# Performance work log

Measured on AMD Instinct MI355X. Metric: run time of the kernel, lower is better.

The kernel has to match this reference:

```python
import jax, jax.numpy as jnp
import numpy as np

N = 100000   # total nodes across the ragged graph batch
E = 800000   # edges
B = 4096     # graphs
V = 103      # element vocab (embedding rows)
D_IN = 200   # embedding dim
H = 256      # hidden dim


def setup_inputs() -> dict:
    key = jax.random.key(0)
    ks = jax.random.split(key, 20)
    s = 0.05
    return {
        "weight": jax.random.normal(ks[0], (V, D_IN), jnp.float32),
        "sto_x": jax.random.randint(ks[1], (N,), 0, V),
        "sto_edge_index": jax.random.randint(ks[2], (2, E), 0, N),
        "sto_weight": jax.random.uniform(ks[3], (N,), jnp.float32),
        "sto_batch": jnp.sort(jax.random.randint(ks[4], (N,), 0, B)),
        "gW0": jax.random.normal(ks[5], (D_IN, H), jnp.float32) * s,
        "gb0": jnp.zeros((H,), jnp.float32),
        "gW1": jax.random.normal(ks[6], (H, H), jnp.float32) * s,
        "gb1": jnp.zeros((H,), jnp.float32),
        "gW2": jax.random.normal(ks[7], (H, H), jnp.float32) * s,
        "gb2": jnp.zeros((H,), jnp.float32),
        "lstm_Wih": jax.random.normal(ks[8], (4 * H, 2 * H), jnp.float32) * s,
        "lstm_Whh": jax.random.normal(ks[9], (4 * H, H), jnp.float32) * s,
        "lstm_bih": jnp.zeros((4 * H,), jnp.float32),
        "lstm_bhh": jnp.zeros((4 * H,), jnp.float32),
        "mlin_W": jax.random.normal(ks[10], (H, 2 * H), jnp.float32) * s,
        "mlin_b": jnp.zeros((H,), jnp.float32),
        "p0W": jax.random.normal(ks[11], (128, H), jnp.float32) * s,
        "p0b": jnp.zeros((128,), jnp.float32),
        "p1W": jax.random.normal(ks[12], (128, 128), jnp.float32) * s,
        "p1b": jnp.zeros((128,), jnp.float32),
        "p2W": jax.random.normal(ks[13], (1, 128), jnp.float32) * s,
        "p2b": jnp.zeros((1,), jnp.float32),
    }


def reference(weight, sto_x, sto_edge_index, sto_weight, sto_batch,
              gW0, gb0, gW1, gb1, gW2, gb2,
              lstm_Wih, lstm_Whh, lstm_bih, lstm_bhh,
              mlin_W, mlin_b, p0W, p0b, p1W, p1b, p2W, p2b):
    # embedding gather (sto_x - 1, with -1 wrapping to the last row as in torch)
    x = weight[sto_x - 1]

    # --- GCN (3 layers, symmetric norm with self-loops, ReLU between layers) ---
    loop = jnp.arange(N)
    src = jnp.concatenate([sto_edge_index[0], loop])
    dst = jnp.concatenate([sto_edge_index[1], loop])
    deg = jax.ops.segment_sum(jnp.ones_like(dst, jnp.float32), dst, N)
    dinv = jax.lax.rsqrt(jnp.maximum(deg, 1.0))
    norm = (dinv[src] * dinv[dst])[:, None]

    def conv(h_in, W, b):
        hw = h_in @ W                                   # [N, H]
        return jax.ops.segment_sum(hw[src] * norm, dst, N) + b

    x = jax.nn.relu(conv(x, gW0, gb0))
    x = jax.nn.relu(conv(x, gW1, gb1))
    x = conv(x, gW2, gb2)

    # --- stoichiometric weighting + graph-wise scatter sum ---
    wx = x * sto_weight[:, None]                        # [N, H]
    sto = jax.ops.segment_sum(wx, sto_batch, B)         # [B, H]

    # --- Set2Set pooling (2 processing steps, 1-layer LSTM) ---
    h = jnp.zeros((B, H), wx.dtype)
    c = jnp.zeros((B, H), wx.dtype)
    q_star = jnp.zeros((B, 2 * H), wx.dtype)
    for _ in range(2):
        gates = q_star @ lstm_Wih.T + lstm_bih + h @ lstm_Whh.T + lstm_bhh
        i, f, g, o = jnp.split(gates, 4, axis=-1)
        c = jax.nn.sigmoid(f) * c + jax.nn.sigmoid(i) * jnp.tanh(g)
        h = jax.nn.sigmoid(o) * jnp.tanh(c)
        e = jnp.sum(wx * h[sto_batch], axis=-1)         # [N]
        emax = jax.ops.segment_max(e, sto_batch, B)
        a = jnp.exp(e - emax[sto_batch])
        a = a / (jax.ops.segment_sum(a, sto_batch, B)[sto_batch] + 1e-16)
        r = jax.ops.segment_sum(wx * a[:, None], sto_batch, B)
        q_star = jnp.concatenate([h, r], axis=-1)

    mean = q_star @ mlin_W.T + mlin_b + sto
    mean = mean / jnp.maximum(jnp.linalg.norm(mean, axis=1, keepdims=True), 1e-12)

    # --- predictor MLP (LeakyReLU slope 0.01) ---
    y = jax.nn.leaky_relu(mean @ p0W.T + p0b)
    y = jax.nn.leaky_relu(y @ p1W.T + p1b)
    return y @ p2W.T + p2b                              # [B, 1]
```

## Files before the change

kernel.cpp:

```cpp
#include <hip/hip_runtime.h>
#include <math.h>

constexpr int Nn  = 100000;
constexpr int Ee  = 800000;
constexpr int Bb  = 4096;
constexpr int Vv  = 103;
constexpr int DIN = 200;
constexpr int Hh  = 256;
constexpr int KV  = 128;

constexpr int SCHUNK = 1024;
constexpr int NSCAN  = (Nn + SCHUNK - 1)/SCHUNK;

using short8 = __attribute__((ext_vector_type(8))) short;
using f32x4  = __attribute__((ext_vector_type(4))) float;

__device__ __forceinline__ float sigf(float x){ return 1.f/(1.f+expf(-x)); }

__device__ __forceinline__ unsigned short f2bf(float f){
  unsigned int u = __float_as_uint(f);
  u += 0x7FFFu + ((u >> 16) & 1u);
  return (unsigned short)(u >> 16);
}
__device__ __forceinline__ float bf2f(unsigned int u){
  return __uint_as_float((u & 0xFFFFu) << 16);
}

__global__ void k_transpose(const float* __restrict__ in, float* __restrict__ out, int R, int C){
  int idx = blockIdx.x*256 + threadIdx.x;
  if (idx >= R*C) return;
  int r = idx / C, c = idx % C;
  out[(size_t)c*R + r] = in[(size_t)r*C + c];
}

__global__ void k_transpose_b(const float* __restrict__ in, unsigned short* __restrict__ out, int R, int C){
  int idx = blockIdx.x*256 + threadIdx.x;
  if (idx >= R*C) return;
  int r = idx / C, c = idx % C;
  out[(size_t)c*R + r] = f2bf(in[(size_t)r*C + c]);
}

__global__ void k_castb(const float* __restrict__ in, unsigned short* __restrict__ out, int n){
  int i = blockIdx.x*256 + threadIdx.x;
  if (i < n) out[i] = f2bf(in[i]);
}

__global__ void k_wg0t(const float* __restrict__ WG0, unsigned short* __restrict__ WG0tb){
  int i = blockIdx.x*256 + threadIdx.x;
  if (i >= Hh*KV) return;
  int n = i >> 7, k = i & (KV-1);
  float v = (k < Vv) ? WG0[(size_t)k*Hh + n] : 0.f;
  WG0tb[i] = f2bf(v);
}

__global__ void k_packW(const float* __restrict__ Wih, const float* __restrict__ Whh,
                        unsigned short* __restrict__ Wp){
  int i = blockIdx.x*256 + threadIdx.x;
  if (i >= 4*Hh*3*Hh) return;
  int g = i / (3*Hh), j = i % (3*Hh);
  float v = (j < 2*Hh) ? Wih[(size_t)g*2*Hh + j] : Whh[(size_t)g*Hh + (j - 2*Hh)];
  Wp[i] = f2bf(v);
}

__global__ void k_count(const int* __restrict__ dst, int* __restrict__ counts){
  int e = blockIdx.x*256 + threadIdx.x;
  if (e < Ee) atomicAdd(&counts[dst[e]], 1);
}

__global__ void k_dinv(const int* __restrict__ counts, float* __restrict__ dinv){
  int n = blockIdx.x*256 + threadIdx.x;
  if (n < Nn) dinv[n] = rsqrtf((float)(counts[n] + 1));
}

__global__ void k_scan1(const int* __restrict__ counts, int* __restrict__ partial){
  __shared__ int red[256];
  int t = threadIdx.x;
  int base = blockIdx.x*SCHUNK + t*4;
  int s = 0;
  if (base + 3 < Nn){ int4 v = *reinterpret_cast<const int4*>(counts + base); s = v.x+v.y+v.z+v.w; }
  else { for (int i=0;i<4;++i) if (base+i<Nn) s += counts[base+i]; }
  red[t] = s; __syncthreads();
  for (int st=128; st>0; st>>=1){ if (t<st) red[t]+=red[t+st]; __syncthreads(); }
  if (t==0) partial[blockIdx.x] = red[0];
}

__global__ void k_scan2(int* __restrict__ partial, int n){
  __shared__ int buf[128];
  int t = threadIdx.x;
  int v = (t < n) ? partial[t] : 0;
  buf[t] = v; __syncthreads();
  for (int off=1; off<128; off<<=1){
    int tv = (t>=off) ? buf[t-off] : 0;
    __syncthreads();
    buf[t] += tv;
    __syncthreads();
  }
  if (t < n) partial[t] = buf[t] - v;
}

__global__ void k_scan3(const int* __restrict__ counts, const int* __restrict__ partial,
                        int* __restrict__ offs){
  __shared__ int red[256];
  int t = threadIdx.x;
  int base = blockIdx.x*SCHUNK + t*4;
  int c0=0,c1=0,c2=0,c3=0;
  if (base + 3 < Nn){ int4 v = *reinterpret_cast<const int4*>(counts + base); c0=v.x;c1=v.y;c2=v.z;c3=v.w; }
  else { if (base<Nn) c0=counts[base]; if (base+1<Nn) c1=counts[base+1];
         if (base+2<Nn) c2=counts[base+2]; if (base+3<Nn) c3=counts[base+3]; }
  int s = c0+c1+c2+c3;
  red[t] = s; __syncthreads();
  for (int off=1; off<256; off<<=1){
    int tv = (t>=off) ? red[t-off] : 0;
    __syncthreads();
    red[t] += tv;
    __syncthreads();
  }
  int run = partial[blockIdx.x] + red[t] - s;
  if (base   < Nn) offs[base]   = run; run += c0;
  if (base+1 < Nn) offs[base+1] = run; run += c1;
  if (base+2 < Nn) offs[base+2] = run; run += c2;
  if (base+3 < Nn) offs[base+3] = run; run += c3;
  if (blockIdx.x == gridDim.x-1 && t == 255) offs[Nn] = partial[blockIdx.x] + red[255];
}

__global__ void k_copyi(const int* __restrict__ a, int* __restrict__ b, int n){
  int i = blockIdx.x*256 + threadIdx.x;
  if (i < n) b[i] = a[i];
}

__global__ void k_fill(const int* __restrict__ ei, const float* __restrict__ dinv,
                       int* __restrict__ fptr, int* __restrict__ srcs, float* __restrict__ norms){
  int e = blockIdx.x*256 + threadIdx.x;
  if (e >= Ee) return;
  int s = ei[e], d = ei[Ee + e];
  int pos = atomicAdd(&fptr[d], 1);
  srcs[pos]  = s;
  norms[pos] = dinv[s]*dinv[d];
}

__global__ void k_boffs(const int* __restrict__ batch, int* __restrict__ boffs){
  int b = blockIdx.x*256 + threadIdx.x;
  if (b > Bb) return;
  int lo = 0, hi = Nn;
  while (lo < hi){ int mid = (lo+hi)>>1; if (batch[mid] < b) lo = mid+1; else hi = mid; }
  boffs[b] = lo;
}

__global__ void k_hist(const int* __restrict__ sto_x, const int* __restrict__ offs,
                       const int* __restrict__ srcs, const float* __restrict__ norms,
                       const float* __restrict__ dinv, unsigned short* __restrict__ Vb){
  __shared__ float hist[4][KV];
  int wid = threadIdx.x >> 6, lane = threadIdx.x & 63;
  int n = blockIdx.x*4 + wid;
  hist[wid][lane] = 0.f; hist[wid][lane+64] = 0.f;
  __syncthreads();
  int s = offs[n], e = offs[n+1];
  for (int k = s + lane; k < e; k += 64){
    int r2 = sto_x[srcs[k]]; r2 = (r2 == 0) ? (Vv-1) : r2-1;
    atomicAdd(&hist[wid][r2], norms[k]);
  }
  if (lane == 0){
    int r0 = sto_x[n]; r0 = (r0 == 0) ? (Vv-1) : r0-1;
    float dn = dinv[n];
    atomicAdd(&hist[wid][r0], dn*dn);
  }
  __syncthreads();
  unsigned int p = ((unsigned int)f2bf(hist[wid][2*lane+1]) << 16) | f2bf(hist[wid][2*lane]);
  ((unsigned int*)Vb)[(size_t)n*(KV/2) + lane] = p;
}

__global__ void k_agg(const unsigned short* __restrict__ Xb, const int* __restrict__ offs,
                      const int* __restrict__ srcs, const float* __restrict__ norms,
                      const float* __restrict__ dinv, unsigned short* __restrict__ T){
  int wid = threadIdx.x >> 6, lane = threadIdx.x & 63;
  int n = blockIdx.x*4 + wid;
  const uint2* Xv = (const uint2*)Xb;
  uint2 v = Xv[(size_t)n*64 + lane];
  float dn = dinv[n]; float s2 = dn*dn;
  float a0 = bf2f(v.x)*s2, a1 = bf2f(v.x>>16)*s2;
  float a2 = bf2f(v.y)*s2, a3 = bf2f(v.y>>16)*s2;
  int s = offs[n], e = offs[n+1];
  int k = s;
  for (; k + 3 < e; k += 4){
    int s0 = srcs[k], s1 = srcs[k+1], s2i = srcs[k+2], s3 = srcs[k+3];
    float n0 = norms[k], n1 = norms[k+1], n2 = norms[k+2], n3 = norms[k+3];
    uint2 g0 = Xv[(size_t)s0*64 + lane];
    uint2 g1 = Xv[(size_t)s1*64 + lane];
    uint2 g2 = Xv[(size_t)s2i*64 + lane];
    uint2 g3 = Xv[(size_t)s3*64 + lane];
    a0 += bf2f(g0.x)*n0; a1 += bf2f(g0.x>>16)*n0; a2 += bf2f(g0.y)*n0; a3 += bf2f(g0.y>>16)*n0;
    a0 += bf2f(g1.x)*n1; a1 += bf2f(g1.x>>16)*n1; a2 += bf2f(g1.y)*n1; a3 += bf2f(g1.y>>16)*n1;
    a0 += bf2f(g2.x)*n2; a1 += bf2f(g2.x>>16)*n2; a2 += bf2f(g2.y)*n2; a3 += bf2f(g2.y>>16)*n2;
    a0 += bf2f(g3.x)*n3; a1 += bf2f(g3.x>>16)*n3; a2 += bf2f(g3.y)*n3; a3 += bf2f(g3.y>>16)*n3;
  }
  for (; k < e; ++k){
    uint2 g0 = Xv[(size_t)srcs[k]*64 + lane];
    float n0 = norms[k];
    a0 += bf2f(g0.x)*n0; a1 += bf2f(g0.x>>16)*n0;
    a2 += bf2f(g0.y)*n0; a3 += bf2f(g0.y>>16)*n0;
  }
  uint2 o;
  o.x = (unsigned int)f2bf(a0) | ((unsigned int)f2bf(a1) << 16);
  o.y = (unsigned int)f2bf(a2) | ((unsigned int)f2bf(a3) << 16);
  ((uint2*)T)[(size_t)n*64 + lane] = o;
}

__global__ __launch_bounds__(512) void k_gemm8(
    const unsigned short* __restrict__ A, int lda,
    const unsigned short* __restrict__ Bt,
    const float* __restrict__ bias, const float* __restrict__ rowscale,
    const float* __restrict__ addf,
    float* __restrict__ Cf, unsigned short* __restrict__ Cb,
    int M, int K, int Nc, int relu)
{
  __shared__ unsigned short lds[18432];
  unsigned short (*Al)[40] = (unsigned short(*)[40])lds;
  unsigned short (*Bl)[40] = (unsigned short(*)[40])(lds + 128*40);

  int tid = threadIdx.x;
  int w = tid >> 6, lane = tid & 63;
  int wr = (w >> 1)*32, wc = (w & 1)*64;
  int l16 = lane & 15, kh = lane >> 4;
  int rbase = blockIdx.y*128, cbase = blockIdx.x*128;
  int sr = tid >> 2, sb = tid & 3;

  f32x4 acc[2][4] = {};

  for (int k0 = 0; k0 < K; k0 += 32){
    int kk = k0 + sb*8;
    uint4 a0 = make_uint4(0,0,0,0);
    int ar0 = rbase + sr;
    if (ar0 < M) a0 = *reinterpret_cast<const uint4*>(A + (size_t)ar0*lda + kk);
    uint4 b0 = *reinterpret_cast<const uint4*>(Bt + (size_t)(cbase + sr)*K + kk);
    __syncthreads();
    *reinterpret_cast<uint4*>(&Al[sr][sb*8]) = a0;
    *reinterpret_cast<uint4*>(&Bl[sr][sb*8]) = b0;
    __syncthreads();

    short8 af[2], bfv[4];
    #pragma unroll
    for (int m = 0; m < 2; ++m) af[m] = *reinterpret_cast<const short8*>(&Al[wr + m*16 + l16][kh*8]);
    #pragma unroll
    for (int n2 = 0; n2 < 4; ++n2) bfv[n2] = *reinterpret_cast<const short8*>(&Bl[wc + n2*16 + l16][kh*8]);
    #pragma unroll
    for (int m = 0; m < 2; ++m)
      #pragma unroll
      for (int n2 = 0; n2 < 4; ++n2)
        acc[m][n2] = __builtin_amdgcn_mfma_f32_16x16x32_bf16(af[m], bfv[n2], acc[m][n2], 0, 0, 0);
  }

  if (Cf){
    #pragma unroll
    for (int n2 = 0; n2 < 4; ++n2){
      int col = cbase + wc + n2*16 + l16;
      float bv = bias ? bias[col] : 0.f;
      #pragma unroll
      for (int m = 0; m < 2; ++m){
        #pragma unroll
        for (int i = 0; i < 4; ++i){
          int row = rbase + wr + m*16 + kh*4 + i;
          if (row >= M) continue;
          float v = acc[m][n2][i] + bv;
          if (addf) v += addf[(size_t)row*Nc + col];
          if (rowscale) v *= rowscale[row];
          if (relu) v = fmaxf(v, 0.f);
          Cf[(size_t)row*Nc + col] = v;
        }
      }
    }
  }
  if (Cb){
    __syncthreads();
    unsigned short* eps = lds + w*(32*72);
    #pragma unroll
    for (int n2 = 0; n2 < 4; ++n2){
      int colg = cbase + wc + n2*16 + l16;
      float bv = bias ? bias[colg] : 0.f;
      #pragma unroll
      for (int m = 0; m < 2; ++m){
        #pragma unroll
        for (int i = 0; i < 4; ++i){
          int lrow = m*16 + kh*4 + i;
          int rowg = rbase + wr + lrow;
          float v = acc[m][n2][i] + bv;
          float rs = (rowscale && rowg < M) ? rowscale[rowg] : 1.f;
          v *= rs;
          if (relu) v = fmaxf(v, 0.f);
          eps[lrow*72 + n2*16 + l16] = f2bf(v);
        }
      }
    }
    int c8 = lane & 7;
    #pragma unroll
    for (int rd = 0; rd < 4; ++rd){
      int lrow = rd*8 + (lane >> 3);
      int rowg = rbase + wr + lrow;
      short8 vv = *reinterpret_cast<const short8*>(&eps[lrow*72 + c8*8]);
      if (rowg < M)
        *reinterpret_cast<short8*>(Cb + (size_t)rowg*Nc + cbase + wc + c8*8) = vv;
    }
  }
}

__global__ __launch_bounds__(256) void k_gemm_nt(
    const float* __restrict__ A, const float* __restrict__ Bt,
    const float* __restrict__ bias, const float* __restrict__ Dadd,
    float* __restrict__ C, int M, int K, int Nc, int accum, int act)
{
  __shared__ float As[64][20];
  __shared__ float Bs[64][20];
  int tid = threadIdx.x;
  int rbase = blockIdx.y*64, cbase = blockIdx.x*64;
  int ty = tid>>4, tx = tid&15;
  int lr = tid>>2, lq = tid&3;
  float acc[4][4] = {};
  for (int k0 = 0; k0 < K; k0 += 16){
    float4 av = make_float4(0,0,0,0), bv = make_float4(0,0,0,0);
    int kk = k0 + lq*4;
    int ar = rbase + lr;
    if (ar < M && kk < K){
      if (kk + 3 < K) av = *reinterpret_cast<const float4*>(A + (size_t)ar*K + kk);
      else { float t0[4] = {0,0,0,0}; for (int i=0; i<4 && kk+i<K; ++i) t0[i] = A[(size_t)ar*K + kk + i];
             av = make_float4(t0[0],t0[1],t0[2],t0[3]); }
    }
    int br = cbase + lr;
    if (br < Nc && kk < K){
      if (kk + 3 < K) bv = *reinterpret_cast<const float4*>(Bt + (size_t)br*K + kk);
      else { float t0[4] = {0,0,0,0}; for (int i=0; i<4 && kk+i<K; ++i) t0[i] = Bt[(size_t)br*K + kk + i];
             bv = make_float4(t0[0],t0[1],t0[2],t0[3]); }
    }
    __syncthreads();
    *reinterpret_cast<float4*>(&As[lr][lq*4]) = av;
    *reinterpret_cast<float4*>(&Bs[lr][lq*4]) = bv;
    __syncthreads();
    #pragma unroll
    for (int kc = 0; kc < 16; kc += 4){
      float4 a4[4], b4[4];
      #pragma unroll
      for (int i=0;i<4;++i) a4[i] = *reinterpret_cast<float4*>(&As[ty*4+i][kc]);
      #pragma unroll
      for (int j=0;j<4;++j) b4[j] = *reinterpret_cast<float4*>(&Bs[tx*4+j][kc]);
      #pragma unroll
      for (int i=0;i<4;++i)
        #pragma unroll
        for (int j=0;j<4;++j)
          acc[i][j] += a4[i].x*b4[j].x + a4[i].y*b4[j].y + a4[i].z*b4[j].z + a4[i].w*b4[j].w;
    }
  }
  #pragma unroll
  for (int i=0;i<4;++i){
    int r = rbase + ty*4 + i;
    if (r >= M) continue;
    #pragma unroll
    for (int j=0;j<4;++j){
      int cc = cbase + tx*4 + j;
      if (cc >= Nc) continue;
      float v = acc[i][j];
      if (accum) v += C[(size_t)r*Nc + cc];
      if (bias)  v += bias[cc];
      if (Dadd)  v += Dadd[(size_t)r*Nc + cc];
      if (act == 1) v = (v > 0.f) ? v : 0.01f*v;
      C[(size_t)r*Nc + cc] = v;
    }
  }
}

__global__ void k_bsum(const float* __restrict__ bih, const float* __restrict__ bhh,
                       float* __restrict__ bsum){
  int g = blockIdx.x*256 + threadIdx.x;
  if (g < 4*Hh) bsum[g] = bih[g] + bhh[g];
}

__global__ void k_lstm(const float* __restrict__ gates, float* __restrict__ cbuf,
                       float* __restrict__ hbuf, unsigned short* __restrict__ qh){
  int idx = blockIdx.x*256 + threadIdx.x;
  if (idx >= Bb*Hh) return;
  int b = idx >> 8, ch = idx & 255;
  const float* g = gates + (size_t)b*4*Hh;
  float ig = sigf(g[ch]);
  float fg = sigf(g[Hh + ch]);
  float gg = tanhf(g[2*Hh + ch]);
  float og = sigf(g[3*Hh + ch]);
  float cn = fg*cbuf[idx] + ig*gg;
  float hn = og*tanhf(cn);
  cbuf[idx] = cn; hbuf[idx] = hn;
  unsigned short hb = f2bf(hn);
  qh[(size_t)b*3*Hh + ch] = hb;
  qh[(size_t)b*3*Hh + 2*Hh + ch] = hb;
}

__global__ void k_pool(const unsigned short* __restrict__ wxb,
                       const float* __restrict__ hbuf,
                       const int* __restrict__ boffs,
                       unsigned short* __restrict__ qh,
                       float* __restrict__ sto, int do_sto){
  int wid = threadIdx.x >> 6, lane = threadIdx.x & 63;
  int g = blockIdx.x*4 + wid;
  if (g >= Bb) return;
  const uint2* Xv = (const uint2*)wxb;
  float4 hv = ((const float4*)hbuf)[(size_t)g*64 + lane];
  int s = boffs[g], e = boffs[g+1];
  float m = -INFINITY, ssum = 0.f;
  float a0=0.f,a1=0.f,a2=0.f,a3=0.f;
  float t0=0.f,t1=0.f,t2=0.f,t3=0.f;
  for (int n = s; n < e; ++n){
    uint2 v = Xv[(size_t)n*64 + lane];
    float x0=bf2f(v.x), x1=bf2f(v.x>>16), x2=bf2f(v.y), x3=bf2f(v.y>>16);
    if (do_sto){ t0+=x0; t1+=x1; t2+=x2; t3+=x3; }
    float d = x0*hv.x + x1*hv.y + x2*hv.z + x3*hv.w;
    #pragma unroll
    for (int mask=32; mask; mask>>=1) d += __shfl_xor(d, mask, 64);
    if (d > m){
      float sc = expf(m - d);
      ssum = ssum*sc + 1.f;
      a0 = a0*sc + x0; a1 = a1*sc + x1; a2 = a2*sc + x2; a3 = a3*sc + x3;
      m = d;
    } else {
      float p = expf(d - m);
      ssum += p;
      a0 += p*x0; a1 += p*x1; a2 += p*x2; a3 += p*x3;
    }
  }
  float inv = 1.f/(ssum + 1e-16f);
  uint2 o;
  o.x = (unsigned int)f2bf(a0*inv) | ((unsigned int)f2bf(a1*inv) << 16);
  o.y = (unsigned int)f2bf(a2*inv) | ((unsigned int)f2bf(a3*inv) << 16);
  ((uint2*)(qh + (size_t)g*3*Hh + Hh))[lane] = o;
  if (do_sto) ((float4*)sto)[(size_t)g*64 + lane] = make_float4(t0,t1,t2,t3);
}

__global__ void k_norm(float* __restrict__ mean){
  __shared__ float red[256];
  int b = blockIdx.x, tid = threadIdx.x;
  float v = mean[(size_t)b*Hh + tid];
  red[tid] = v*v; __syncthreads();
  for (int st=128; st>0; st>>=1){ if (tid<st) red[tid] += red[tid+st]; __syncthreads(); }
  float nrm = fmaxf(sqrtf(red[0]), 1e-12f);
  mean[(size_t)b*Hh + tid] = v/nrm;
}

__global__ void k_out(const float* __restrict__ y1, const float* __restrict__ p2W,
                      const float* __restrict__ p2b, float* __restrict__ out){
  __shared__ float red[128];
  int b = blockIdx.x, tid = threadIdx.x;
  float v = y1[(size_t)b*128 + tid]*p2W[tid];
  red[tid] = v; __syncthreads();
  for (int st=64; st>0; st>>=1){ if (tid<st) red[tid] += red[tid+st]; __syncthreads(); }
  if (tid == 0) out[b] = red[0] + p2b[0];
}

extern "C" void kernel_launch(void* const* d_in, const int* in_sizes, int n_in,
                              void* d_out, int out_size, void* d_ws, size_t ws_size,
                              hipStream_t stream) {
  const float* weight   = (const float*)d_in[0];
  const int*   sto_x    = (const int*)  d_in[1];
  const int*   ei       = (const int*)  d_in[2];
  const float* sto_w    = (const float*)d_in[3];
  const int*   batch    = (const int*)  d_in[4];
  const float* gW0 = (const float*)d_in[5];   const float* gb0 = (const float*)d_in[6];
  const float* gW1 = (const float*)d_in[7];   const float* gb1 = (const float*)d_in[8];
  const float* gW2 = (const float*)d_in[9];   const float* gb2 = (const float*)d_in[10];
  const float* Wih = (const float*)d_in[11];  const float* Whh = (const float*)d_in[12];
  const float* bih = (const float*)d_in[13];  const float* bhh = (const float*)d_in[14];
  const float* mW  = (const float*)d_in[15];  const float* mb  = (const float*)d_in[16];
  const float* p0W = (const float*)d_in[17];  const float* p0b = (const float*)d_in[18];
  const float* p1W = (const float*)d_in[19];  const float* p1b = (const float*)d_in[20];
  const float* p2W = (const float*)d_in[21];  const float* p2b = (const float*)d_in[22];
  float* out = (float*)d_out;

  char* w = (char*)d_ws;
  auto alloc = [&](size_t bytes)->char*{ char* p = w; w += (bytes + 255) & ~size_t(255); return p; };
  unsigned short* Xb = (unsigned short*)alloc((size_t)Nn*Hh*2);
  unsigned short* Tb = (unsigned short*)alloc((size_t)Nn*Hh*2);
  unsigned short* Vb = (unsigned short*)alloc((size_t)Nn*KV*2);
  float* WG0   = (float*)alloc((size_t)Vv*Hh*4);
  unsigned short* WG0tb = (unsigned short*)alloc((size_t)Hh*KV*2);
  float* gW0t  = (float*)alloc((size_t)Hh*DIN*4);
  unsigned short* gW1tb = (unsigned short*)alloc((size_t)Hh*Hh*2);
  unsigned short* gW2tb = (unsigned short*)alloc((size_t)Hh*Hh*2);
  unsigned short* Wpb   = (unsigned short*)alloc((size_t)4*Hh*3*Hh*2);
  unsigned short* mWb   = (unsigned short*)alloc((size_t)Hh*2*Hh*2);
  int*   counts= (int*)  alloc((size_t)Nn*4);
  int*   offs  = (int*)  alloc((size_t)(Nn+1)*4);
  int*   fptr  = (int*)  alloc((size_t)Nn*4);
  int*   spart = (int*)  alloc((size_t)NSCAN*4);
  float* dinv  = (float*)alloc((size_t)Nn*4);
  int*   srcs  = (int*)  alloc((size_t)Ee*4);
  float* norms = (float*)alloc((size_t)Ee*4);
  int*   boffs = (int*)  alloc((size_t)(Bb+1)*4);
  float* sto   = (float*)alloc((size_t)Bb*Hh*4);
  float* hbuf  = (float*)alloc((size_t)Bb*Hh*4);
  float* cbuf  = (float*)alloc((size_t)Bb*Hh*4);
  unsigned short* qh = (unsigned short*)alloc((size_t)Bb*3*Hh*2);
  float* gates = (float*)alloc((size_t)Bb*4*Hh*4);
  float* bsum  = (float*)alloc((size_t)4*Hh*4);
  float* meanb = (float*)alloc((size_t)Bb*Hh*4);
  float* y0    = (float*)alloc((size_t)Bb*128*4);
  float* y1    = (float*)alloc((size_t)Bb*128*4);

  auto gemm = [&](const float* A, const float* Bt, const float* bias, const float* Dadd,
                  float* C, int M, int K, int Nc, int accum, int act){
    dim3 g((Nc+63)/64, (M+63)/64);
    k_gemm_nt<<<g, 256, 0, stream>>>(A, Bt, bias, Dadd, C, M, K, Nc, accum, act);
  };
  auto gemm8 = [&](const unsigned short* A, int lda, const unsigned short* Bt,
                   const float* bias, const float* rowscale, const float* addf,
                   float* Cf, unsigned short* Cb, int M, int K, int Nc, int relu){
    dim3 g(Nc/128, (M+127)/128);
    k_gemm8<<<g, 512, 0, stream>>>(A, lda, Bt, bias, rowscale, addf, Cf, Cb, M, K, Nc, relu);
  };

  hipMemsetAsync(counts, 0, (size_t)Nn*4, stream);
  hipMemsetAsync(cbuf,  0, (size_t)Bb*Hh*4, stream);
  hipMemsetAsync(qh,    0, (size_t)Bb*3*Hh*2, stream);

  k_transpose<<<(DIN*Hh+255)/256, 256, 0, stream>>>(gW0, gW0t, DIN, Hh);
  k_transpose_b<<<(Hh*Hh+255)/256, 256, 0, stream>>>(gW1, gW1tb, Hh, Hh);
  k_transpose_b<<<(Hh*Hh+255)/256, 256, 0, stream>>>(gW2, gW2tb, Hh, Hh);
  k_packW<<<(4*Hh*3*Hh+255)/256, 256, 0, stream>>>(Wih, Whh, Wpb);
  k_castb<<<(Hh*2*Hh+255)/256, 256, 0, stream>>>(mW, mWb, Hh*2*Hh);

  k_count<<<(Ee+255)/256, 256, 0, stream>>>(ei + Ee, counts);
  k_dinv<<<(Nn+255)/256, 256, 0, stream>>>(counts, dinv);
  k_scan1<<<NSCAN, 256, 0, stream>>>(counts, spart);
  k_scan2<<<1, 128, 0, stream>>>(spart, NSCAN);
  k_scan3<<<NSCAN, 256, 0, stream>>>(counts, spart, offs);
  k_copyi<<<(Nn+255)/256, 256, 0, stream>>>(offs, fptr, Nn);
  k_fill<<<(Ee+255)/256, 256, 0, stream>>>(ei, dinv, fptr, srcs, norms);
  k_boffs<<<(Bb+256)/256, 256, 0, stream>>>(batch, boffs);

  gemm(weight, gW0t, nullptr, nullptr, WG0, Vv, DIN, Hh, 0, 0);
  k_wg0t<<<(Hh*KV+255)/256, 256, 0, stream>>>(WG0, WG0tb);
  k_hist<<<Nn/4, 256, 0, stream>>>(sto_x, offs, srcs, norms, dinv, Vb);
  gemm8(Vb, KV, WG0tb, gb0, nullptr, nullptr, nullptr, Xb, Nn, KV, Hh, 1);

  k_agg<<<Nn/4, 256, 0, stream>>>(Xb, offs, srcs, norms, dinv, Tb);
  gemm8(Tb, Hh, gW1tb, gb1, nullptr, nullptr, nullptr, Xb, Nn, Hh, Hh, 1);
  k_agg<<<Nn/4, 256, 0, stream>>>(Xb, offs, srcs, norms, dinv, Tb);
  gemm8(Tb, Hh, gW2tb, gb2, sto_w, nullptr, nullptr, Xb, Nn, Hh, Hh, 0);

  k_bsum<<<(4*Hh+255)/256, 256, 0, stream>>>(bih, bhh, bsum);

  for (int t = 0; t < 2; ++t){
    gemm8(qh, 3*Hh, Wpb, bsum, nullptr, nullptr, gates, nullptr, Bb, 3*Hh, 4*Hh, 0);
    k_lstm<<<(Bb*Hh+255)/256, 256, 0, stream>>>(gates, cbuf, hbuf, qh);
    k_pool<<<Bb/4, 256, 0, stream>>>(Xb, hbuf, boffs, qh, sto, t == 0);
  }

  gemm8(qh, 3*Hh, mWb, mb, nullptr, sto, meanb, nullptr, Bb, 2*Hh, Hh, 0);
  k_norm<<<Bb, Hh, 0, stream>>>(meanb);
  gemm(meanb, p0W, p0b, nullptr, y0, Bb, Hh, 128, 0, 1);
  gemm(y0, p1W, p1b, nullptr, y1, Bb, 128, 128, 0, 1);
  k_out<<<Bb, 128, 0, stream>>>(y1, p2W, p2b, out);
}
```

Measured before the change: 593.0 us.

## Fuse GCN aggregation with layer GEMM, pack edge records, move MLP to bf16 MFMA

Merges the neighbor aggregation and the following dense 256x256 GEMM into one kernel for GCN layers 2 and 3. Each block aggregates 64 rows into LDS and multiplies them with MFMA, so the bf16 intermediate T no longer makes a round trip through global memory. Edge source index and norm are packed into one uint2 so each edge needs a single load. The predictor MLP now runs through the bf16 MFMA GEMM with a LeakyReLU mode instead of fp32 GEMMs, which costs some precision in that head. The fused kernel reads its B operand straight from global memory (L2) rather than staging it in LDS.

```diff
diff --git a/kernel.cpp b/kernel.cpp
--- a/kernel.cpp
+++ b/kernel.cpp
@@ -129,13 +129,12 @@
 }
 
 __global__ void k_fill(const int* __restrict__ ei, const float* __restrict__ dinv,
-                       int* __restrict__ fptr, int* __restrict__ srcs, float* __restrict__ norms){
+                       int* __restrict__ fptr, uint2* __restrict__ epack){
   int e = blockIdx.x*256 + threadIdx.x;
   if (e >= Ee) return;
   int s = ei[e], d = ei[Ee + e];
   int pos = atomicAdd(&fptr[d], 1);
-  srcs[pos]  = s;
-  norms[pos] = dinv[s]*dinv[d];
+  epack[pos] = make_uint2((unsigned int)s, __float_as_uint(dinv[s]*dinv[d]));
 }
 
 __global__ void k_boffs(const int* __restrict__ batch, int* __restrict__ boffs){
@@ -147,8 +146,8 @@
 }
 
 __global__ void k_hist(const int* __restrict__ sto_x, const int* __restrict__ offs,
-                       const int* __restrict__ srcs, const float* __restrict__ norms,
-                       const float* __restrict__ dinv, unsigned short* __restrict__ Vb){
+                       const uint2* __restrict__ epack, const float* __restrict__ dinv,
+                       unsigned short* __restrict__ Vb){
   __shared__ float hist[4][KV];
   int wid = threadIdx.x >> 6, lane = threadIdx.x & 63;
   int n = blockIdx.x*4 + wid;
@@ -156,8 +155,9 @@
   __syncthreads();
   int s = offs[n], e = offs[n+1];
   for (int k = s + lane; k < e; k += 64){
-    int r2 = sto_x[srcs[k]]; r2 = (r2 == 0) ? (Vv-1) : r2-1;
-    atomicAdd(&hist[wid][r2], norms[k]);
+    uint2 ev = epack[k];
+    int r2 = sto_x[ev.x]; r2 = (r2 == 0) ? (Vv-1) : r2-1;
+    atomicAdd(&hist[wid][r2], __uint_as_float(ev.y));
   }
   if (lane == 0){
     int r0 = sto_x[n]; r0 = (r0 == 0) ? (Vv-1) : r0-1;
@@ -169,40 +169,111 @@
   ((unsigned int*)Vb)[(size_t)n*(KV/2) + lane] = p;
 }
 
-__global__ void k_agg(const unsigned short* __restrict__ Xb, const int* __restrict__ offs,
-                      const int* __restrict__ srcs, const float* __restrict__ norms,
-                      const float* __restrict__ dinv, unsigned short* __restrict__ T){
-  int wid = threadIdx.x >> 6, lane = threadIdx.x & 63;
-  int n = blockIdx.x*4 + wid;
+__global__ __launch_bounds__(512, 4) void k_conv_fused(
+    const unsigned short* __restrict__ Xb,
+    const uint2* __restrict__ epack,
+    const int* __restrict__ offs,
+    const float* __restrict__ dinv,
+    const unsigned short* __restrict__ Bt,
+    const float* __restrict__ bias,
+    const float* __restrict__ sw,
+    unsigned short* __restrict__ Cb,
+    int M, int relu)
+{
+  __shared__ unsigned short lds[18432];
+  unsigned short (*Tl)[264] = (unsigned short(*)[264])lds;
+
+  int tid = threadIdx.x;
+  int w = tid >> 6, lane = tid & 63;
+  int rbase = blockIdx.x * 64;
   const uint2* Xv = (const uint2*)Xb;
-  uint2 v = Xv[(size_t)n*64 + lane];
-  float dn = dinv[n]; float s2 = dn*dn;
-  float a0 = bf2f(v.x)*s2, a1 = bf2f(v.x>>16)*s2;
-  float a2 = bf2f(v.y)*s2, a3 = bf2f(v.y>>16)*s2;
-  int s = offs[n], e = offs[n+1];
-  int k = s;
-  for (; k + 3 < e; k += 4){
-    int s0 = srcs[k], s1 = srcs[k+1], s2i = srcs[k+2], s3 = srcs[k+3];
-    float n0 = norms[k], n1 = norms[k+1], n2 = norms[k+2], n3 = norms[k+3];
-    uint2 g0 = Xv[(size_t)s0*64 + lane];
-    uint2 g1 = Xv[(size_t)s1*64 + lane];
-    uint2 g2 = Xv[(size_t)s2i*64 + lane];
-    uint2 g3 = Xv[(size_t)s3*64 + lane];
-    a0 += bf2f(g0.x)*n0; a1 += bf2f(g0.x>>16)*n0; a2 += bf2f(g0.y)*n0; a3 += bf2f(g0.y>>16)*n0;
-    a0 += bf2f(g1.x)*n1; a1 += bf2f(g1.x>>16)*n1; a2 += bf2f(g1.y)*n1; a3 += bf2f(g1.y>>16)*n1;
-    a0 += bf2f(g2.x)*n2; a1 += bf2f(g2.x>>16)*n2; a2 += bf2f(g2.y)*n2; a3 += bf2f(g2.y>>16)*n2;
-    a0 += bf2f(g3.x)*n3; a1 += bf2f(g3.x>>16)*n3; a2 += bf2f(g3.y)*n3; a3 += bf2f(g3.y>>16)*n3;
-  }
-  for (; k < e; ++k){
-    uint2 g0 = Xv[(size_t)srcs[k]*64 + lane];
-    float n0 = norms[k];
-    a0 += bf2f(g0.x)*n0; a1 += bf2f(g0.x>>16)*n0;
-    a2 += bf2f(g0.y)*n0; a3 += bf2f(g0.y>>16)*n0;
-  }
-  uint2 o;
-  o.x = (unsigned int)f2bf(a0) | ((unsigned int)f2bf(a1) << 16);
-  o.y = (unsigned int)f2bf(a2) | ((unsigned int)f2bf(a3) << 16);
-  ((uint2*)T)[(size_t)n*64 + lane] = o;
+
+  for (int i = 0; i < 8; ++i){
+    int lr = w*8 + i;
+    int n = rbase + lr;
+    if (n >= M) break;
+    float dn = dinv[n]; float s2 = dn*dn;
+    uint2 v = Xv[(size_t)n*64 + lane];
+    float a0 = bf2f(v.x)*s2, a1 = bf2f(v.x>>16)*s2;
+    float a2 = bf2f(v.y)*s2, a3 = bf2f(v.y>>16)*s2;
+    int s = offs[n], e = offs[n+1];
+    int k = s;
+    for (; k + 3 < e; k += 4){
+      uint2 e0 = epack[k], e1 = epack[k+1], e2 = epack[k+2], e3 = epack[k+3];
+      uint2 g0 = Xv[(size_t)e0.x*64 + lane];
+      uint2 g1 = Xv[(size_t)e1.x*64 + lane];
+      uint2 g2 = Xv[(size_t)e2.x*64 + lane];
+      uint2 g3 = Xv[(size_t)e3.x*64 + lane];
+      float n0 = __uint_as_float(e0.y), n1 = __uint_as_float(e1.y);
+      float n2 = __uint_as_float(e2.y), n3 = __uint_as_float(e3.y);
+      a0 += bf2f(g0.x)*n0; a1 += bf2f(g0.x>>16)*n0; a2 += bf2f(g0.y)*n0; a3 += bf2f(g0.y>>16)*n0;
+      a0 += bf2f(g1.x)*n1; a1 += bf2f(g1.x>>16)*n1; a2 += bf2f(g1.y)*n1; a3 += bf2f(g1.y>>16)*n1;
+      a0 += bf2f(g2.x)*n2; a1 += bf2f(g2.x>>16)*n2; a2 += bf2f(g2.y)*n2; a3 += bf2f(g2.y>>16)*n2;
+      a0 += bf2f(g3.x)*n3; a1 += bf2f(g3.x>>16)*n3; a2 += bf2f(g3.y)*n3; a3 += bf2f(g3.y>>16)*n3;
+    }
+    for (; k < e; ++k){
+      uint2 e0 = epack[k];
+      uint2 g0 = Xv[(size_t)e0.x*64 + lane];
+      float n0 = __uint_as_float(e0.y);
+      a0 += bf2f(g0.x)*n0; a1 += bf2f(g0.x>>16)*n0;
+      a2 += bf2f(g0.y)*n0; a3 += bf2f(g0.y>>16)*n0;
+    }
+    uint2 o;
+    o.x = (unsigned int)f2bf(a0) | ((unsigned int)f2bf(a1) << 16);
+    o.y = (unsigned int)f2bf(a2) | ((unsigned int)f2bf(a3) << 16);
+    *reinterpret_cast<uint2*>(&Tl[lr][lane*4]) = o;
+  }
+  __syncthreads();
+
+  int l16 = lane & 15, kh = lane >> 4;
+  int wr = (w >> 2)*32, wc = (w & 3)*64;
+  f32x4 acc[2][4] = {};
+  const unsigned short* bp0 = Bt + (size_t)(wc + l16)*256 + kh*8;
+
+  #pragma unroll
+  for (int kk = 0; kk < 8; ++kk){
+    short8 af0 = *reinterpret_cast<const short8*>(&Tl[wr + l16][kk*32 + kh*8]);
+    short8 af1 = *reinterpret_cast<const short8*>(&Tl[wr + 16 + l16][kk*32 + kh*8]);
+    short8 bs[4];
+    #pragma unroll
+    for (int f = 0; f < 4; ++f)
+      bs[f] = *reinterpret_cast<const short8*>(bp0 + (size_t)f*16*256 + kk*32);
+    #pragma unroll
+    for (int f = 0; f < 4; ++f){
+      acc[0][f] = __builtin_amdgcn_mfma_f32_16x16x32_bf16(af0, bs[f], acc[0][f], 0, 0, 0);
+      acc[1][f] = __builtin_amdgcn_mfma_f32_16x16x32_bf16(af1, bs[f], acc[1][f], 0, 0, 0);
+    }
+  }
+  __syncthreads();
+
+  unsigned short* eps = lds + w*(32*72);
+  #pragma unroll
+  for (int n2 = 0; n2 < 4; ++n2){
+    int col = wc + n2*16 + l16;
+    float bv = bias[col];
+    #pragma unroll
+    for (int m = 0; m < 2; ++m){
+      #pragma unroll
+      for (int i = 0; i < 4; ++i){
+        int lrow = m*16 + kh*4 + i;
+        int rowg = rbase + wr + lrow;
+        float v = acc[m][n2][i] + bv;
+        float rs = (sw && rowg < M) ? sw[rowg] : 1.f;
+        v *= rs;
+        if (relu) v = fmaxf(v, 0.f);
+        eps[lrow*72 + n2*16 + l16] = f2bf(v);
+      }
+    }
+  }
+  int c8 = lane & 7;
+  #pragma unroll
+  for (int rd = 0; rd < 4; ++rd){
+    int lrow = rd*8 + (lane >> 3);
+    int rowg = rbase + wr + lrow;
+    short8 vv = *reinterpret_cast<const short8*>(&eps[lrow*72 + c8*8]);
+    if (rowg < M)
+      *reinterpret_cast<short8*>(Cb + (size_t)rowg*256 + wc + c8*8) = vv;
+  }
 }
 
 __global__ __launch_bounds__(512) void k_gemm8(
@@ -263,7 +334,8 @@
           float v = acc[m][n2][i] + bv;
           if (addf) v += addf[(size_t)row*Nc + col];
           if (rowscale) v *= rowscale[row];
-          if (relu) v = fmaxf(v, 0.f);
+          if (relu == 1) v = fmaxf(v, 0.f);
+          else if (relu == 2) v = (v > 0.f) ? v : 0.01f*v;
           Cf[(size_t)row*Nc + col] = v;
         }
       }
@@ -285,7 +357,8 @@
           float v = acc[m][n2][i] + bv;
           float rs = (rowscale && rowg < M) ? rowscale[rowg] : 1.f;
           v *= rs;
-          if (relu) v = fmaxf(v, 0.f);
+          if (relu == 1) v = fmaxf(v, 0.f);
+          else if (relu == 2) v = (v > 0.f) ? v : 0.01f*v;
           eps[lrow*72 + n2*16 + l16] = f2bf(v);
         }
       }
@@ -429,14 +502,15 @@
   if (do_sto) ((float4*)sto)[(size_t)g*64 + lane] = make_float4(t0,t1,t2,t3);
 }
 
-__global__ void k_norm(float* __restrict__ mean){
+__global__ void k_norm(float* __restrict__ mean, unsigned short* __restrict__ outb){
   __shared__ float red[256];
   int b = blockIdx.x, tid = threadIdx.x;
   float v = mean[(size_t)b*Hh + tid];
   red[tid] = v*v; __syncthreads();
   for (int st=128; st>0; st>>=1){ if (tid<st) red[tid] += red[tid+st]; __syncthreads(); }
   float nrm = fmaxf(sqrtf(red[0]), 1e-12f);
-  mean[(size_t)b*Hh + tid] = v/nrm;
+  float o = v/nrm;
+  outb[(size_t)b*Hh + tid] = f2bf(o);
 }
 
 __global__ void k_out(const float* __restrict__ y1, const float* __restrict__ p2W,
@@ -470,8 +544,8 @@
 
   char* w = (char*)d_ws;
   auto alloc = [&](size_t bytes)->char*{ char* p = w; w += (bytes + 255) & ~size_t(255); return p; };
-  unsigned short* Xb = (unsigned short*)alloc((size_t)Nn*Hh*2);
-  unsigned short* Tb = (unsigned short*)alloc((size_t)Nn*Hh*2);
+  unsigned short* X1 = (unsigned short*)alloc((size_t)Nn*Hh*2);
+  unsigned short* X2 = (unsigned short*)alloc((size_t)Nn*Hh*2);
   unsigned short* Vb = (unsigned short*)alloc((size_t)Nn*KV*2);
   float* WG0   = (float*)alloc((size_t)Vv*Hh*4);
   unsigned short* WG0tb = (unsigned short*)alloc((size_t)Hh*KV*2);
@@ -480,13 +554,14 @@
   unsigned short* gW2tb = (unsigned short*)alloc((size_t)Hh*Hh*2);
   unsigned short* Wpb   = (unsigned short*)alloc((size_t)4*Hh*3*Hh*2);
   unsigned short* mWb   = (unsigned short*)alloc((size_t)Hh*2*Hh*2);
+  unsigned short* p0Wb  = (unsigned short*)alloc((size_t)128*Hh*2);
+  unsigned short* p1Wb  = (unsigned short*)alloc((size_t)128*128*2);
   int*   counts= (int*)  alloc((size_t)Nn*4);
   int*   offs  = (int*)  alloc((size_t)(Nn+1)*4);
   int*   fptr  = (int*)  alloc((size_t)Nn*4);
   int*   spart = (int*)  alloc((size_t)NSCAN*4);
   float* dinv  = (float*)alloc((size_t)Nn*4);
-  int*   srcs  = (int*)  alloc((size_t)Ee*4);
-  float* norms = (float*)alloc((size_t)Ee*4);
+  uint2* epack = (uint2*)alloc((size_t)Ee*8);
   int*   boffs = (int*)  alloc((size_t)(Bb+1)*4);
   float* sto   = (float*)alloc((size_t)Bb*Hh*4);
   float* hbuf  = (float*)alloc((size_t)Bb*Hh*4);
@@ -495,7 +570,8 @@
   float* gates = (float*)alloc((size_t)Bb*4*Hh*4);
   float* bsum  = (float*)alloc((size_t)4*Hh*4);
   float* meanb = (float*)alloc((size_t)Bb*Hh*4);
-  float* y0    = (float*)alloc((size_t)Bb*128*4);
+  unsigned short* meanbb = (unsigned short*)alloc((size_t)Bb*Hh*2);
+  unsigned short* y0b = (unsigned short*)alloc((size_t)Bb*128*2);
   float* y1    = (float*)alloc((size_t)Bb*128*4);
 
   auto gemm = [&](const float* A, const float* Bt, const float* bias, const float* Dadd,
@@ -519,6 +595,8 @@
   k_transpose_b<<<(Hh*Hh+255)/256, 256, 0, stream>>>(gW2, gW2tb, Hh, Hh);
   k_packW<<<(4*Hh*3*Hh+255)/256, 256, 0, stream>>>(Wih, Whh, Wpb);
   k_castb<<<(Hh*2*Hh+255)/256, 256, 0, stream>>>(mW, mWb, Hh*2*Hh);
+  k_castb<<<(128*Hh+255)/256, 256, 0, stream>>>(p0W, p0Wb, 128*Hh);
+  k_castb<<<(128*128+255)/256, 256, 0, stream>>>(p1W, p1Wb, 128*128);
 
   k_count<<<(Ee+255)/256, 256, 0, stream>>>(ei + Ee, counts);
   k_dinv<<<(Nn+255)/256, 256, 0, stream>>>(counts, dinv);
@@ -526,30 +604,28 @@
   k_scan2<<<1, 128, 0, stream>>>(spart, NSCAN);
   k_scan3<<<NSCAN, 256, 0, stream>>>(counts, spart, offs);
   k_copyi<<<(Nn+255)/256, 256, 0, stream>>>(offs, fptr, Nn);
-  k_fill<<<(Ee+255)/256, 256, 0, stream>>>(ei, dinv, fptr, srcs, norms);
+  k_fill<<<(Ee+255)/256, 256, 0, stream>>>(ei, dinv, fptr, epack);
   k_boffs<<<(Bb+256)/256, 256, 0, stream>>>(batch, boffs);
 
   gemm(weight, gW0t, nullptr, nullptr, WG0, Vv, DIN, Hh, 0, 0);
   k_wg0t<<<(Hh*KV+255)/256, 256, 0, stream>>>(WG0, WG0tb);
-  k_hist<<<Nn/4, 256, 0, stream>>>(sto_x, offs, srcs, norms, dinv, Vb);
-  gemm8(Vb, KV, WG0tb, gb0, nullptr, nullptr, nullptr, Xb, Nn, KV, Hh, 1);
-
-  k_agg<<<Nn/4, 256, 0, stream>>>(Xb, offs, srcs, norms, dinv, Tb);
-  gemm8(Tb, Hh, gW1tb, gb1, nullptr, nullptr, nullptr, Xb, Nn, Hh, Hh, 1);
-  k_agg<<<Nn/4, 256, 0, stream>>>(Xb, offs, srcs, norms, dinv, Tb);
-  gemm8(Tb, Hh, gW2tb, gb2, sto_w, nullptr, nullptr, Xb, Nn, Hh, Hh, 0);
+  k_hist<<<Nn/4, 256, 0, stream>>>(sto_x, offs, epack, dinv, Vb);
+  gemm8(Vb, KV, WG0tb, gb0, nullptr, nullptr, nullptr, X1, Nn, KV, Hh, 1);
+
+  k_conv_fused<<<(Nn+63)/64, 512, 0, stream>>>(X1, epack, offs, dinv, gW1tb, gb1, nullptr, X2, Nn, 1);
+  k_conv_fused<<<(Nn+63)/64, 512, 0, stream>>>(X2, epack, offs, dinv, gW2tb, gb2, sto_w, X1, Nn, 0);
 
   k_bsum<<<(4*Hh+255)/256, 256, 0, stream>>>(bih, bhh, bsum);
 
   for (int t = 0; t < 2; ++t){
     gemm8(qh, 3*Hh, Wpb, bsum, nullptr, nullptr, gates, nullptr, Bb, 3*Hh, 4*Hh, 0);
     k_lstm<<<(Bb*Hh+255)/256, 256, 0, stream>>>(gates, cbuf, hbuf, qh);
-    k_pool<<<Bb/4, 256, 0, stream>>>(Xb, hbuf, boffs, qh, sto, t == 0);
+    k_pool<<<Bb/4, 256, 0, stream>>>(X1, hbuf, boffs, qh, sto, t == 0);
   }
 
   gemm8(qh, 3*Hh, mWb, mb, nullptr, sto, meanb, nullptr, Bb, 2*Hh, Hh, 0);
-  k_norm<<<Bb, Hh, 0, stream>>>(meanb);
-  gemm(meanb, p0W, p0b, nullptr, y0, Bb, Hh, 128, 0, 1);
-  gemm(y0, p1W, p1b, nullptr, y1, Bb, 128, 128, 0, 1);
+  k_norm<<<Bb, Hh, 0, stream>>>(meanb, meanbb);
+  gemm8(meanbb, Hh, p0Wb, p0b, nullptr, nullptr, nullptr, y0b, Bb, Hh, 128, 2);
+  gemm8(y0b, 128, p1Wb, p1b, nullptr, nullptr, y1, nullptr, Bb, 128, 128, 2);
   k_out<<<Bb, 128, 0, stream>>>(y1, p2W, p2b, out);
 }
```

After: 688.4 us. 16.1% more time.

## Pack edge src/norm into uint2, unroll aggregation by 8, bf16 MFMA predictor MLP

Applied to the files above, without the earlier changes.

Source index and normalization weight are interleaved into one 8-byte record, so the aggregation and histogram kernels issue one load per edge instead of two. The aggregation loop now prefetches 8 edges and their feature gathers per iteration to raise memory-level parallelism. The two predictor MLP layers move from the fp32 GEMM to the bf16 MFMA GEMM, which gains a LeakyReLU mode; the normalized mean is written as bf16 and two extra weight casts are added. This lowers precision in the head and adds register pressure in the aggregation kernel.

```diff
diff --git a/kernel.cpp b/kernel.cpp
--- a/kernel.cpp
+++ b/kernel.cpp
@@ -129,13 +129,12 @@
 }
 
 __global__ void k_fill(const int* __restrict__ ei, const float* __restrict__ dinv,
-                       int* __restrict__ fptr, int* __restrict__ srcs, float* __restrict__ norms){
+                       int* __restrict__ fptr, uint2* __restrict__ epack){
   int e = blockIdx.x*256 + threadIdx.x;
   if (e >= Ee) return;
   int s = ei[e], d = ei[Ee + e];
   int pos = atomicAdd(&fptr[d], 1);
-  srcs[pos]  = s;
-  norms[pos] = dinv[s]*dinv[d];
+  epack[pos] = make_uint2((unsigned int)s, __float_as_uint(dinv[s]*dinv[d]));
 }
 
 __global__ void k_boffs(const int* __restrict__ batch, int* __restrict__ boffs){
@@ -147,8 +146,8 @@
 }
 
 __global__ void k_hist(const int* __restrict__ sto_x, const int* __restrict__ offs,
-                       const int* __restrict__ srcs, const float* __restrict__ norms,
-                       const float* __restrict__ dinv, unsigned short* __restrict__ Vb){
+                       const uint2* __restrict__ epack, const float* __restrict__ dinv,
+                       unsigned short* __restrict__ Vb){
   __shared__ float hist[4][KV];
   int wid = threadIdx.x >> 6, lane = threadIdx.x & 63;
   int n = blockIdx.x*4 + wid;
@@ -156,8 +155,9 @@
   __syncthreads();
   int s = offs[n], e = offs[n+1];
   for (int k = s + lane; k < e; k += 64){
-    int r2 = sto_x[srcs[k]]; r2 = (r2 == 0) ? (Vv-1) : r2-1;
-    atomicAdd(&hist[wid][r2], norms[k]);
+    uint2 ev = epack[k];
+    int r2 = sto_x[ev.x]; r2 = (r2 == 0) ? (Vv-1) : r2-1;
+    atomicAdd(&hist[wid][r2], __uint_as_float(ev.y));
   }
   if (lane == 0){
     int r0 = sto_x[n]; r0 = (r0 == 0) ? (Vv-1) : r0-1;
@@ -170,8 +170,8 @@
 }
 
 __global__ void k_agg(const unsigned short* __restrict__ Xb, const int* __restrict__ offs,
-                      const int* __restrict__ srcs, const float* __restrict__ norms,
-                      const float* __restrict__ dinv, unsigned short* __restrict__ T){
+                      const uint2* __restrict__ epack, const float* __restrict__ dinv,
+                      unsigned short* __restrict__ T){
   int wid = threadIdx.x >> 6, lane = threadIdx.x & 63;
   int n = blockIdx.x*4 + wid;
   const uint2* Xv = (const uint2*)Xb;
@@ -181,21 +181,31 @@
   float a2 = bf2f(v.y)*s2, a3 = bf2f(v.y>>16)*s2;
   int s = offs[n], e = offs[n+1];
   int k = s;
-  for (; k + 3 < e; k += 4){
-    int s0 = srcs[k], s1 = srcs[k+1], s2i = srcs[k+2], s3 = srcs[k+3];
-    float n0 = norms[k], n1 = norms[k+1], n2 = norms[k+2], n3 = norms[k+3];
-    uint2 g0 = Xv[(size_t)s0*64 + lane];
-    uint2 g1 = Xv[(size_t)s1*64 + lane];
-    uint2 g2 = Xv[(size_t)s2i*64 + lane];
-    uint2 g3 = Xv[(size_t)s3*64 + lane];
+  for (; k + 7 < e; k += 8){
+    uint2 ev[8], g[8];
+    #pragma unroll
+    for (int j = 0; j < 8; ++j) ev[j] = epack[k+j];
+    #pragma unroll
+    for (int j = 0; j < 8; ++j) g[j] = Xv[(size_t)ev[j].x*64 + lane];
+    #pragma unroll
+    for (int j = 0; j < 8; ++j){
+      float nn = __uint_as_float(ev[j].y);
+      a0 += bf2f(g[j].x)*nn; a1 += bf2f(g[j].x>>16)*nn;
+      a2 += bf2f(g[j].y)*nn; a3 += bf2f(g[j].y>>16)*nn;
+    }
+  }
+  for (; k + 1 < e; k += 2){
+    uint2 e0 = epack[k], e1 = epack[k+1];
+    uint2 g0 = Xv[(size_t)e0.x*64 + lane];
+    uint2 g1 = Xv[(size_t)e1.x*64 + lane];
+    float n0 = __uint_as_float(e0.y), n1 = __uint_as_float(e1.y);
     a0 += bf2f(g0.x)*n0; a1 += bf2f(g0.x>>16)*n0; a2 += bf2f(g0.y)*n0; a3 += bf2f(g0.y>>16)*n0;
     a0 += bf2f(g1.x)*n1; a1 += bf2f(g1.x>>16)*n1; a2 += bf2f(g1.y)*n1; a3 += bf2f(g1.y>>16)*n1;
-    a0 += bf2f(g2.x)*n2; a1 += bf2f(g2.x>>16)*n2; a2 += bf2f(g2.y)*n2; a3 += bf2f(g2.y>>16)*n2;
-    a0 += bf2f(g3.x)*n3; a1 += bf2f(g3.x>>16)*n3; a2 += bf2f(g3.y)*n3; a3 += bf2f(g3.y>>16)*n3;
-  }
-  for (; k < e; ++k){
-    uint2 g0 = Xv[(size_t)srcs[k]*64 + lane];
-    float n0 = norms[k];
+  }
+  if (k < e){
+    uint2 e0 = epack[k];
+    uint2 g0 = Xv[(size_t)e0.x*64 + lane];
+    float n0 = __uint_as_float(e0.y);
     a0 += bf2f(g0.x)*n0; a1 += bf2f(g0.x>>16)*n0;
     a2 += bf2f(g0.y)*n0; a3 += bf2f(g0.y>>16)*n0;
   }
@@ -263,7 +273,8 @@
           float v = acc[m][n2][i] + bv;
           if (addf) v += addf[(size_t)row*Nc + col];
           if (rowscale) v *= rowscale[row];
-          if (relu) v = fmaxf(v, 0.f);
+          if (relu == 1) v = fmaxf(v, 0.f);
+          else if (relu == 2) v = (v > 0.f) ? v : 0.01f*v;
           Cf[(size_t)row*Nc + col] = v;
         }
       }
@@ -285,7 +296,8 @@
           float v = acc[m][n2][i] + bv;
           float rs = (rowscale && rowg < M) ? rowscale[rowg] : 1.f;
           v *= rs;
-          if (relu) v = fmaxf(v, 0.f);
+          if (relu == 1) v = fmaxf(v, 0.f);
+          else if (relu == 2) v = (v > 0.f) ? v : 0.01f*v;
           eps[lrow*72 + n2*16 + l16] = f2bf(v);
         }
       }
@@ -429,14 +441,15 @@
   if (do_sto) ((float4*)sto)[(size_t)g*64 + lane] = make_float4(t0,t1,t2,t3);
 }
 
-__global__ void k_norm(float* __restrict__ mean){
+__global__ void k_norm(float* __restrict__ mean, unsigned short* __restrict__ outb){
   __shared__ float red[256];
   int b = blockIdx.x, tid = threadIdx.x;
   float v = mean[(size_t)b*Hh + tid];
   red[tid] = v*v; __syncthreads();
   for (int st=128; st>0; st>>=1){ if (tid<st) red[tid] += red[tid+st]; __syncthreads(); }
   float nrm = fmaxf(sqrtf(red[0]), 1e-12f);
-  mean[(size_t)b*Hh + tid] = v/nrm;
+  float o = v/nrm;
+  outb[(size_t)b*Hh + tid] = f2bf(o);
 }
 
 __global__ void k_out(const float* __restrict__ y1, const float* __restrict__ p2W,
@@ -480,13 +493,14 @@
   unsigned short* gW2tb = (unsigned short*)alloc((size_t)Hh*Hh*2);
   unsigned short* Wpb   = (unsigned short*)alloc((size_t)4*Hh*3*Hh*2);
   unsigned short* mWb   = (unsigned short*)alloc((size_t)Hh*2*Hh*2);
+  unsigned short* p0Wb  = (unsigned short*)alloc((size_t)128*Hh*2);
+  unsigned short* p1Wb  = (unsigned short*)alloc((size_t)128*128*2);
   int*   counts= (int*)  alloc((size_t)Nn*4);
   int*   offs  = (int*)  alloc((size_t)(Nn+1)*4);
   int*   fptr  = (int*)  alloc((size_t)Nn*4);
   int*   spart = (int*)  alloc((size_t)NSCAN*4);
   float* dinv  = (float*)alloc((size_t)Nn*4);
-  int*   srcs  = (int*)  alloc((size_t)Ee*4);
-  float* norms = (float*)alloc((size_t)Ee*4);
+  uint2* epack = (uint2*)alloc((size_t)Ee*8);
   int*   boffs = (int*)  alloc((size_t)(Bb+1)*4);
   float* sto   = (float*)alloc((size_t)Bb*Hh*4);
   float* hbuf  = (float*)alloc((size_t)Bb*Hh*4);
@@ -495,7 +509,8 @@
   float* gates = (float*)alloc((size_t)Bb*4*Hh*4);
   float* bsum  = (float*)alloc((size_t)4*Hh*4);
   float* meanb = (float*)alloc((size_t)Bb*Hh*4);
-  float* y0    = (float*)alloc((size_t)Bb*128*4);
+  unsigned short* meanbb = (unsigned short*)alloc((size_t)Bb*Hh*2);
+  unsigned short* y0b = (unsigned short*)alloc((size_t)Bb*128*2);
   float* y1    = (float*)alloc((size_t)Bb*128*4);
 
   auto gemm = [&](const float* A, const float* Bt, const float* bias, const float* Dadd,
@@ -519,6 +534,8 @@
   k_transpose_b<<<(Hh*Hh+255)/256, 256, 0, stream>>>(gW2, gW2tb, Hh, Hh);
   k_packW<<<(4*Hh*3*Hh+255)/256, 256, 0, stream>>>(Wih, Whh, Wpb);
   k_castb<<<(Hh*2*Hh+255)/256, 256, 0, stream>>>(mW, mWb, Hh*2*Hh);
+  k_castb<<<(128*Hh+255)/256, 256, 0, stream>>>(p0W, p0Wb, 128*Hh);
+  k_castb<<<(128*128+255)/256, 256, 0, stream>>>(p1W, p1Wb, 128*128);
 
   k_count<<<(Ee+255)/256, 256, 0, stream>>>(ei + Ee, counts);
   k_dinv<<<(Nn+255)/256, 256, 0, stream>>>(counts, dinv);
@@ -526,17 +543,17 @@
   k_scan2<<<1, 128, 0, stream>>>(spart, NSCAN);
   k_scan3<<<NSCAN, 256, 0, stream>>>(counts, spart, offs);
   k_copyi<<<(Nn+255)/256, 256, 0, stream>>>(offs, fptr, Nn);
-  k_fill<<<(Ee+255)/256, 256, 0, stream>>>(ei, dinv, fptr, srcs, norms);
+  k_fill<<<(Ee+255)/256, 256, 0, stream>>>(ei, dinv, fptr, epack);
   k_boffs<<<(Bb+256)/256, 256, 0, stream>>>(batch, boffs);
 
   gemm(weight, gW0t, nullptr, nullptr, WG0, Vv, DIN, Hh, 0, 0);
   k_wg0t<<<(Hh*KV+255)/256, 256, 0, stream>>>(WG0, WG0tb);
-  k_hist<<<Nn/4, 256, 0, stream>>>(sto_x, offs, srcs, norms, dinv, Vb);
+  k_hist<<<Nn/4, 256, 0, stream>>>(sto_x, offs, epack, dinv, Vb);
   gemm8(Vb, KV, WG0tb, gb0, nullptr, nullptr, nullptr, Xb, Nn, KV, Hh, 1);
 
-  k_agg<<<Nn/4, 256, 0, stream>>>(Xb, offs, srcs, norms, dinv, Tb);
+  k_agg<<<Nn/4, 256, 0, stream>>>(Xb, offs, epack, dinv, Tb);
   gemm8(Tb, Hh, gW1tb, gb1, nullptr, nullptr, nullptr, Xb, Nn, Hh, Hh, 1);
-  k_agg<<<Nn/4, 256, 0, stream>>>(Xb, offs, srcs, norms, dinv, Tb);
+  k_agg<<<Nn/4, 256, 0, stream>>>(Xb, offs, epack, dinv, Tb);
   gemm8(Tb, Hh, gW2tb, gb2, sto_w, nullptr, nullptr, Xb, Nn, Hh, Hh, 0);
 
   k_bsum<<<(4*Hh+255)/256, 256, 0, stream>>>(bih, bhh, bsum);
@@ -548,8 +565,8 @@
   }
 
   gemm8(qh, 3*Hh, mWb, mb, nullptr, sto, meanb, nullptr, Bb, 2*Hh, Hh, 0);
-  k_norm<<<Bb, Hh, 0, stream>>>(meanb);
-  gemm(meanb, p0W, p0b, nullptr, y0, Bb, Hh, 128, 0, 1);
-  gemm(y0, p1W, p1b, nullptr, y1, Bb, 128, 128, 0, 1);
+  k_norm<<<Bb, Hh, 0, stream>>>(meanb, meanbb);
+  gemm8(meanbb, Hh, p0Wb, p0b, nullptr, nullptr, nullptr, y0b, Bb, Hh, 128, 2);
+  gemm8(y0b, 128, p1Wb, p1b, nullptr, nullptr, y1, nullptr, Bb, 128, 128, 2);
   k_out<<<Bb, 128, 0, stream>>>(y1, p2W, p2b, out);
 }
```

After: 567.8 us. 1.04x faster.
